# Kernel optimization log

Hardware: AMD Instinct MI355X
Metric: run time of the kernel (lower is better)

Reference implementation:

```python
import jax, jax.numpy as jnp
import numpy as np
from jax import lax

EPS = 1e-8

def squash(x, axis=-1):
    sq = jnp.sum(x * x, axis=axis, keepdims=True)
    return sq / (1.0 + sq) * x / (jnp.sqrt(sq) + EPS)

def setup_inputs() -> dict:
    key = jax.random.key(0)
    ks = jax.random.split(key, 12)
    B = 512
    x = jax.random.normal(ks[0], (B, 1, 28, 28), dtype=jnp.float32)
    conv1_w = 0.05 * jax.random.normal(ks[1], (256, 1, 9, 9), dtype=jnp.float32)
    conv1_b = jnp.zeros((256,), dtype=jnp.float32)
    prim_w = 0.01 * jax.random.normal(ks[2], (256, 256, 9, 9), dtype=jnp.float32)
    prim_b = jnp.zeros((256,), dtype=jnp.float32)
    # DigitCaps W: (out_caps=10, in_caps=1152, out_dim=16, in_dim=8)
    W_digit = 0.01 * jax.random.normal(ks[3], (10, 1152, 16, 8), dtype=jnp.float32)
    dec_w1 = 0.05 * jax.random.normal(ks[4], (512, 160), dtype=jnp.float32)
    dec_b1 = jnp.zeros((512,), dtype=jnp.float32)
    dec_w2 = 0.05 * jax.random.normal(ks[5], (1024, 512), dtype=jnp.float32)
    dec_b2 = jnp.zeros((1024,), dtype=jnp.float32)
    dec_w3 = 0.05 * jax.random.normal(ks[6], (784, 1024), dtype=jnp.float32)
    dec_b3 = jnp.zeros((784,), dtype=jnp.float32)
    return {"x": x, "conv1_w": conv1_w, "conv1_b": conv1_b,
            "prim_w": prim_w, "prim_b": prim_b, "W_digit": W_digit,
            "dec_w1": dec_w1, "dec_b1": dec_b1, "dec_w2": dec_w2,
            "dec_b2": dec_b2, "dec_w3": dec_w3, "dec_b3": dec_b3}

def reference(x, conv1_w, conv1_b, prim_w, prim_b, W_digit,
              dec_w1, dec_b1, dec_w2, dec_b2, dec_w3, dec_b3):
    NUM_ROUTING = 3
    # conv1 + relu: [B,1,28,28] -> [B,256,20,20]
    out = lax.conv(x, conv1_w, (1, 1), 'VALID') + conv1_b[None, :, None, None]
    out = jax.nn.relu(out)
    # primary caps conv: -> [B,256,6,6]
    out = lax.conv(out, prim_w, (2, 2), 'VALID') + prim_b[None, :, None, None]
    N, C, H, W = out.shape
    # [B,32,8,6,6] -> [B,32,6,6,8] -> [B,1152,8]
    out = out.reshape(N, 32, 8, H, W).transpose(0, 1, 3, 4, 2).reshape(N, -1, 8)
    u = squash(out)
    # u_hat: [B, out_caps=10, in_caps=1152, out_dim=16]
    u_hat = jnp.einsum('ocdi,bci->bocd', W_digit, u)
    tu = lax.stop_gradient(u_hat)
    b = jnp.zeros((N, 10, 1152, 1), dtype=u_hat.dtype)
    for _ in range(NUM_ROUTING - 1):
        c = jax.nn.softmax(b, axis=1)
        s = jnp.sum(c * tu, axis=2)            # [B,10,16]
        v = squash(s)
        b = b + jnp.einsum('bocd,bod->boc', tu, v)[..., None]
    c = jax.nn.softmax(b, axis=1)
    s = jnp.sum(c * u_hat, axis=2)
    v = squash(s)                               # [B,10,16]
    logits = jnp.linalg.norm(v, axis=-1)        # [B,10]
    pred = jax.nn.one_hot(jnp.argmax(logits, axis=1), 10, dtype=v.dtype)  # [B,10]
    masked = (v * pred[..., None]).reshape(N, -1)  # [B,160]
    h = jax.nn.relu(masked @ dec_w1.T + dec_b1)
    h = jax.nn.relu(h @ dec_w2.T + dec_b2)
    reconstruction = jax.nn.sigmoid(h @ dec_w3.T + dec_b3)  # [B,784]
    return (logits, reconstruction)
```

## Files before the change

### kernel.cpp

```cpp
#include <hip/hip_runtime.h>
#include <math.h>

typedef unsigned short u16;
typedef unsigned int u32;
typedef __attribute__((ext_vector_type(4))) float f32x4;
typedef __attribute__((ext_vector_type(4))) u32 u32x4;
typedef __attribute__((ext_vector_type(8))) short s16x8;
typedef __attribute__((ext_vector_type(8))) u16 u16x8;

__device__ __forceinline__ float bf2f(u16 h) { return __uint_as_float(((u32)h) << 16); }
__device__ __forceinline__ u16 f2bf(float f) {
    u32 u = __float_as_uint(f);
    return (u16)((u + 0x7FFFu + ((u >> 16) & 1u)) >> 16);
}
__device__ __forceinline__ void unpack8(u16x8 a, float* f) {
    const u32* p = (const u32*)&a;
#pragma unroll
    for (int k = 0; k < 4; ++k) {
        u32 w = p[k];
        f[2 * k] = __uint_as_float(w << 16);
        f[2 * k + 1] = __uint_as_float(w & 0xffff0000u);
    }
}

#define OFF_CONV1 0ull
#define OFF_CP    104857600ull
#define OFF_UHAT  0ull
#define OFF_U     188743680ull
#define OFF_WR    198180864ull
#define OFF_WB    208797696ull
#define OFF_W1T   211746816ull
#define OFF_MASK  211829760ull
#define OFF_H1    212157440ull
#define OFF_H2    213206016ull

#define GLDS16(SRC, DST) __builtin_amdgcn_global_load_lds( \
    (const __attribute__((address_space(1))) unsigned int*)(SRC), \
    (__attribute__((address_space(3))) unsigned int*)(DST), 16, 0, 0)

__global__ void k_w1t(const float* __restrict__ cw, float* __restrict__ w1t) {
    int k = blockIdx.x, t = threadIdx.x;
    w1t[k * 256 + t] = cw[t * 81 + k];
}

__global__ void k_wr(const float* __restrict__ pw, u16* __restrict__ wr) {
    int och = blockIdx.x, t = threadIdx.x;
    const float* src = pw + (och * 256 + t) * 81;
    u16* dst = wr + (size_t)och * 20736 + t;
    for (int kk = 0; kk < 81; ++kk) dst[kk * 256] = f2bf(src[kk]);
}

__global__ void k_wb(const float* __restrict__ w, u16* __restrict__ o) {
    int i = (blockIdx.x * 256 + threadIdx.x) * 8;
    u16x8 r;
#pragma unroll
    for (int j = 0; j < 8; ++j) r[j] = f2bf(w[i + j]);
    *(u16x8*)&o[i] = r;
}

__global__ __launch_bounds__(256) void k_conv1(const float* __restrict__ x,
                                               const float* __restrict__ w1t,
                                               const float* __restrict__ bias,
                                               u16* __restrict__ out) {
    int b = blockIdx.x / 20, y = blockIdx.x % 20, t = threadIdx.x;
    __shared__ float xs[252];
    if (t < 252) xs[t] = x[b * 784 + y * 28 + t];
    __syncthreads();
    float acc[20];
#pragma unroll
    for (int i = 0; i < 20; ++i) acc[i] = 0.f;
#pragma unroll
    for (int ky = 0; ky < 9; ++ky) {
        float xr[28];
#pragma unroll
        for (int i = 0; i < 28; ++i) xr[i] = xs[ky * 28 + i];
#pragma unroll
        for (int kx = 0; kx < 9; ++kx) {
            float wv = w1t[(ky * 9 + kx) * 256 + t];
#pragma unroll
            for (int ox = 0; ox < 20; ++ox) acc[ox] += wv * xr[ox + kx];
        }
    }
    float bv = bias[t];
    u16* op = out + ((size_t)(b * 20 + y) * 20) * 256 + t;
#pragma unroll
    for (int ox = 0; ox < 20; ++ox) {
        float f = fmaxf(acc[ox] + bv, 0.f);
        op[ox * 256] = f2bf(f);
    }
}

__global__ __launch_bounds__(256) void k_gemm(const u16* __restrict__ wr,
                                              const u16* __restrict__ cin,
                                              float* __restrict__ cp) {
    __shared__ __align__(16) u16 Al[128 * 64];
    __shared__ __align__(16) u16 Bl[128 * 64];
    int tid = threadIdx.x, lane = tid & 63, w = tid >> 6;
    int pix0 = blockIdx.x * 128, och0 = blockIdx.y * 128, q = blockIdx.z;
    int kbase = q * 5184;
    int slot = lane & 7;
    const char* ab[4];
    const char* bb[4];
#pragma unroll
    for (int j = 0; j < 4; ++j) {
        int r = w * 32 + j * 8 + (lane >> 3);
        int sl = slot ^ (r & 7);
        ab[j] = (const char*)wr + (size_t)(och0 + r) * 41472 + sl * 16;
        int p = pix0 + r, bi = p / 36, rr = p % 36, yy = rr / 6, xx = rr % 6;
        bb[j] = (const char*)cin + (size_t)((bi * 20 + 2 * yy) * 20 + 2 * xx) * 512 + sl * 16;
    }
    f32x4 acc[4][4];
#pragma unroll
    for (int i = 0; i < 4; ++i)
#pragma unroll
        for (int j = 0; j < 4; ++j) acc[i][j] = (f32x4){0.f, 0.f, 0.f, 0.f};
    int wm = (w & 1) * 64, wn = (w >> 1) * 64;

    for (int it = 0; it < 81; ++it) {
        int kk0 = kbase + it * 64;
        int kykx = kk0 >> 8, ic0 = kk0 & 255;
        int aoffu = kk0 * 2;
        int boffu = ((kykx / 9) * 20 + (kykx % 9)) * 512 + ic0 * 2;
#pragma unroll
        for (int j = 0; j < 4; ++j) {
            GLDS16(ab[j] + aoffu, &Al[(w * 32 + j * 8) * 64]);
            GLDS16(bb[j] + boffu, &Bl[(w * 32 + j * 8) * 64]);
        }
        __syncthreads();
#pragma unroll
        for (int s = 0; s < 2; ++s) {
            s16x8 af[4], bf[4];
#pragma unroll
            for (int f = 0; f < 4; ++f) {
                int m = wm + f * 16 + (lane & 15);
                int ch = ((s << 2) + (lane >> 4)) ^ (m & 7);
                af[f] = *(const s16x8*)&Al[m * 64 + ch * 8];
                int n = wn + f * 16 + (lane & 15);
                int ch2 = ((s << 2) + (lane >> 4)) ^ (n & 7);
                bf[f] = *(const s16x8*)&Bl[n * 64 + ch2 * 8];
            }
#pragma unroll
            for (int fm = 0; fm < 4; ++fm)
#pragma unroll
                for (int fn = 0; fn < 4; ++fn)
                    acc[fm][fn] = __builtin_amdgcn_mfma_f32_16x16x32_bf16(
                        af[fm], bf[fn], acc[fm][fn], 0, 0, 0);
        }
        __syncthreads();
    }
#pragma unroll
    for (int fm = 0; fm < 4; ++fm) {
        int och = och0 + wm + fm * 16 + (lane >> 4) * 4;
#pragma unroll
        for (int fn = 0; fn < 4; ++fn) {
            int pix = pix0 + wn + fn * 16 + (lane & 15);
            *(f32x4*)&cp[(((size_t)q * 18432 + pix) << 8) + och] = acc[fm][fn];
        }
    }
}

__global__ void k_squash(const float* __restrict__ cp, const float* __restrict__ pbias,
                         u16* __restrict__ u) {
    int idx = blockIdx.x * 256 + threadIdx.x;
    int pix = idx >> 5, g = idx & 31;
    size_t base = ((size_t)pix << 8) + g * 8;
    f32x4 s0 = {0.f, 0.f, 0.f, 0.f}, s1 = {0.f, 0.f, 0.f, 0.f};
#pragma unroll
    for (int q = 0; q < 4; ++q) {
        s0 += *(const f32x4*)&cp[q * 4718592ull + base];
        s1 += *(const f32x4*)&cp[q * 4718592ull + base + 4];
    }
    s0 += *(const f32x4*)&pbias[g * 8];
    s1 += *(const f32x4*)&pbias[g * 8 + 4];
    float sq = s0.x * s0.x + s0.y * s0.y + s0.z * s0.z + s0.w * s0.w +
               s1.x * s1.x + s1.y * s1.y + s1.z * s1.z + s1.w * s1.w;
    float scale = (sq / (1.f + sq)) / (sqrtf(sq) + 1e-8f);
    int b = pix / 36, cap = g * 36 + pix % 36;
    u16x8 r;
    r[0] = f2bf(s0.x * scale); r[1] = f2bf(s0.y * scale);
    r[2] = f2bf(s0.z * scale); r[3] = f2bf(s0.w * scale);
    r[4] = f2bf(s1.x * scale); r[5] = f2bf(s1.y * scale);
    r[6] = f2bf(s1.z * scale); r[7] = f2bf(s1.w * scale);
    *(u16x8*)&u[((size_t)b * 1152 + cap) * 8] = r;
}

__global__ __launch_bounds__(256) void k_uhat(const u16* __restrict__ u,
                                              const u16* __restrict__ wb,
                                              u32* __restrict__ uhp) {
    int o = blockIdx.x, cg = blockIdx.y, bq = blockIdx.z, t = threadIdx.x;
    __shared__ __align__(16) u16 wl[64 * 136];
    const u16* wsrc = wb + ((size_t)o * 1152 + cg * 64) * 128;
    for (int i = t; i < 1024; i += 256) {
        int row = i >> 4, j = i & 15;
        *(u16x8*)&wl[row * 136 + j * 8] = *(const u16x8*)&wsrc[i * 8];
    }
    __syncthreads();
    int bl = t >> 5, c2l = t & 31;
    const u16* w0p = &wl[(2 * c2l) * 136];
    const u16* w1p = &wl[(2 * c2l + 1) * 136];
    for (int bt = bq * 16; bt < bq * 16 + 16; ++bt) {
        int b = bt * 8 + bl;
        const u16x8* up = (const u16x8*)(u + ((size_t)b * 1152 + cg * 64 + 2 * c2l) * 8);
        float u0[8], u1[8];
        unpack8(up[0], u0);
        unpack8(up[1], u1);
        u32 outv[16];
#pragma unroll
        for (int d = 0; d < 16; ++d) {
            u16x8 wv0 = *(const u16x8*)&w0p[d * 8];
            u16x8 wv1 = *(const u16x8*)&w1p[d * 8];
            float w0f[8], w1f[8];
            unpack8(wv0, w0f);
            unpack8(wv1, w1f);
            float dA = 0.f, dB = 0.f;
#pragma unroll
            for (int i = 0; i < 8; ++i) {
                dA += w0f[i] * u0[i];
                dB += w1f[i] * u1[i];
            }
            outv[d] = (u32)f2bf(dA) | ((u32)f2bf(dB) << 16);
        }
        u32* dst = uhp + (size_t)b * 92160 + (cg * 32 + c2l) * 160 + o * 16;
#pragma unroll
        for (int k = 0; k < 4; ++k)
            *(u32x4*)&dst[k * 4] = *(u32x4*)&outv[k * 4];
    }
}

__global__ __launch_bounds__(256, 2) void k_routing(const u32* __restrict__ uhp,
                                                    float* __restrict__ logits,
                                                    float* __restrict__ masked) {
    int b = blockIdx.x, t = threadIdx.x;
    __shared__ float blog[10][1160];
    __shared__ __align__(16) u32 chunk[32 * 164];
    __shared__ float cwl[10][66];
    __shared__ float v[160];
    __shared__ float lg[10];
    __shared__ int am;
    for (int i = t; i < 11600; i += 256) ((float*)blog)[i] = 0.f;
    const u32* uh = uhp + (size_t)b * 92160;
    int o16 = t >> 4, d16 = t & 15;
    float s = 0.f;
    __syncthreads();

    if (t < 160) {
        const u32* p = uh + t;
#pragma unroll 8
        for (int c2 = 0; c2 < 576; ++c2) {
            u32 wv = p[c2 * 160];
            s += bf2f((u16)(wv & 0xffffu)) + bf2f((u16)(wv >> 16));
        }
        s *= 0.1f;
        float sq = s * s;
        sq += __shfl_xor(sq, 1, 16);
        sq += __shfl_xor(sq, 2, 16);
        sq += __shfl_xor(sq, 4, 16);
        sq += __shfl_xor(sq, 8, 16);
        float scale = (sq / (1.f + sq)) / (sqrtf(sq) + 1e-8f);
        v[t] = s * scale;
    }
    __syncthreads();

    for (int pass = 1; pass < 3; ++pass) {
        float snew = 0.f;
        for (int cg = 0; cg < 18; ++cg) {
            const u32x4* src4 = (const u32x4*)(uh + (size_t)cg * 5120);
#pragma unroll
            for (int k = 0; k < 5; ++k) {
                int idx4 = t + k * 256;
                int c2l = idx4 / 40, j4 = idx4 - c2l * 40;
                ((u32x4*)chunk)[c2l * 41 + j4] = src4[idx4];
            }
            __syncthreads();
#pragma unroll
            for (int jj = 0; jj < 2; ++jj) {
                int idx = t + jj * 256;
                if (idx < 320) {
                    int c2l = idx / 10, o = idx - c2l * 10;
                    const u32* row = &chunk[c2l * 164 + o * 16];
                    const float* vp = &v[o * 16];
                    float d0 = 0.f, d1 = 0.f;
#pragma unroll
                    for (int d = 0; d < 16; ++d) {
                        u32 wv = row[d];
                        float vv = vp[d];
                        d0 += __uint_as_float(wv << 16) * vv;
                        d1 += __uint_as_float(wv & 0xffff0000u) * vv;
                    }
                    int c2 = cg * 32 + c2l;
                    blog[o][2 * c2] += d0;
                    blog[o][2 * c2 + 1] += d1;
                }
            }
            __syncthreads();
            if (t < 64) {
                int c = cg * 64 + t;
                float bb[10], mx = -1e30f;
#pragma unroll
                for (int o = 0; o < 10; ++o) { bb[o] = blog[o][c]; mx = fmaxf(mx, bb[o]); }
                float sum = 0.f;
#pragma unroll
                for (int o = 0; o < 10; ++o) { bb[o] = __expf(bb[o] - mx); sum += bb[o]; }
                float rs = 1.f / sum;
#pragma unroll
                for (int o = 0; o < 10; ++o) cwl[o][t] = bb[o] * rs;
            }
            __syncthreads();
            if (t < 160) {
                const u32* col = &chunk[t];
                const float* cwp = &cwl[o16][0];
#pragma unroll 8
                for (int c2l = 0; c2l < 32; ++c2l) {
                    u32 wv = col[c2l * 164];
                    snew += __uint_as_float(wv << 16) * cwp[2 * c2l] +
                            __uint_as_float(wv & 0xffff0000u) * cwp[2 * c2l + 1];
                }
            }
            __syncthreads();
        }
        if (t < 160) {
            s = snew;
            float sq = s * s;
            sq += __shfl_xor(sq, 1, 16);
            sq += __shfl_xor(sq, 2, 16);
            sq += __shfl_xor(sq, 4, 16);
            sq += __shfl_xor(sq, 8, 16);
            float scale = (sq / (1.f + sq)) / (sqrtf(sq) + 1e-8f);
            v[t] = s * scale;
            if (d16 == 0 && pass == 2) {
                float sn = sqrtf(sq);
                float l = (sq / (1.f + sq)) * (sn / (sn + 1e-8f));
                lg[o16] = l;
                logits[b * 10 + o16] = l;
            }
        }
        __syncthreads();
    }
    if (t == 0) {
        float best = lg[0];
        int bi = 0;
#pragma unroll
        for (int o = 1; o < 10; ++o)
            if (lg[o] > best) { best = lg[o]; bi = o; }
        am = bi;
    }
    __syncthreads();
    if (t < 160) masked[b * 160 + t] = (o16 == am) ? v[t] : 0.f;
}

template <int K, int OUTDIM, int ACT>
__global__ __launch_bounds__(256) void k_dec(const float* __restrict__ in,
                                             const float* __restrict__ W,
                                             const float* __restrict__ bias,
                                             float* __restrict__ out) {
    int bt = blockIdx.y * 8;
    int o = blockIdx.x * 256 + threadIdx.x;
    __shared__ float ins[8 * K];
    for (int i = threadIdx.x; i < 8 * K; i += 256) ins[i] = in[(size_t)bt * K + i];
    __syncthreads();
    if (o < OUTDIM) {
        float acc[8];
#pragma unroll
        for (int bb = 0; bb < 8; ++bb) acc[bb] = 0.f;
        const float* wr = W + (size_t)o * K;
#pragma unroll 4
        for (int k = 0; k < K; ++k) {
            float wv = wr[k];
#pragma unroll
            for (int bb = 0; bb < 8; ++bb) acc[bb] += wv * ins[bb * K + k];
        }
        float bv = bias[o];
#pragma unroll
        for (int bb = 0; bb < 8; ++bb) {
            float z = acc[bb] + bv;
            float r = (ACT == 0) ? fmaxf(z, 0.f) : 1.f / (1.f + __expf(-z));
            out[(size_t)(bt + bb) * OUTDIM + o] = r;
        }
    }
}

extern "C" void kernel_launch(void* const* d_in, const int* in_sizes, int n_in,
                              void* d_out, int out_size, void* d_ws, size_t ws_size,
                              hipStream_t stream) {
    const float* x       = (const float*)d_in[0];
    const float* conv1_w = (const float*)d_in[1];
    const float* conv1_b = (const float*)d_in[2];
    const float* prim_w  = (const float*)d_in[3];
    const float* prim_b  = (const float*)d_in[4];
    const float* W_digit = (const float*)d_in[5];
    const float* dec_w1  = (const float*)d_in[6];
    const float* dec_b1  = (const float*)d_in[7];
    const float* dec_w2  = (const float*)d_in[8];
    const float* dec_b2  = (const float*)d_in[9];
    const float* dec_w3  = (const float*)d_in[10];
    const float* dec_b3  = (const float*)d_in[11];

    char* ws = (char*)d_ws;
    u16*   conv1o = (u16*)(ws + OFF_CONV1);
    float* cp     = (float*)(ws + OFF_CP);
    u32*   uhat   = (u32*)(ws + OFF_UHAT);
    u16*   u      = (u16*)(ws + OFF_U);
    u16*   wrq    = (u16*)(ws + OFF_WR);
    u16*   wb     = (u16*)(ws + OFF_WB);
    float* w1t    = (float*)(ws + OFF_W1T);
    float* maskd  = (float*)(ws + OFF_MASK);
    float* h1     = (float*)(ws + OFF_H1);
    float* h2     = (float*)(ws + OFF_H2);
    float* logits = (float*)d_out;
    float* recon  = (float*)d_out + 5120;

    k_w1t<<<dim3(81), dim3(256), 0, stream>>>(conv1_w, w1t);
    k_wr<<<dim3(256), dim3(256), 0, stream>>>(prim_w, wrq);
    k_wb<<<dim3(720), dim3(256), 0, stream>>>(W_digit, wb);
    k_conv1<<<dim3(10240), dim3(256), 0, stream>>>(x, w1t, conv1_b, conv1o);
    k_gemm<<<dim3(144, 2, 4), dim3(256), 0, stream>>>(wrq, conv1o, cp);
    k_squash<<<dim3(2304), dim3(256), 0, stream>>>(cp, prim_b, u);
    k_uhat<<<dim3(10, 18, 4), dim3(256), 0, stream>>>(u, wb, uhat);
    k_routing<<<dim3(512), dim3(256), 0, stream>>>(uhat, logits, maskd);
    k_dec<160, 512, 0><<<dim3(2, 64), dim3(256), 0, stream>>>(maskd, dec_w1, dec_b1, h1);
    k_dec<512, 1024, 0><<<dim3(4, 64), dim3(256), 0, stream>>>(h1, dec_w2, dec_b2, h2);
    k_dec<1024, 784, 1><<<dim3(4, 64), dim3(256), 0, stream>>>(h2, dec_w3, dec_b3, recon);
}
```

Baseline: 803.4 us.

## Double-buffer primary-caps GEMM LDS, halve split-K, and coalesce weight repack

The primary-caps GEMM now keeps two LDS buffers and issues the global-to-LDS loads for the next K-slice while MFMAs run on the current one, so load latency overlaps with compute. The split-K factor drops from 4 to 2: each block covers twice the K range, and squash reads and sums only two partial buffers, which cuts partial-sum write and read traffic. The weight repack kernel now stages through shared memory so both its global reads and writes are coalesced. The trade-offs are half as many GEMM blocks (576), which may leave CUs underused, and double the LDS per block (64KB), which limits occupancy.

```diff
diff --git a/kernel.cpp b/kernel.cpp
--- a/kernel.cpp
+++ b/kernel.cpp
@@ -43,11 +43,24 @@
     w1t[k * 256 + t] = cw[t * 81 + k];
 }
 
-__global__ void k_wr(const float* __restrict__ pw, u16* __restrict__ wr) {
+__global__ __launch_bounds__(256) void k_wr(const float* __restrict__ pw,
+                                            u16* __restrict__ wrq) {
     int och = blockIdx.x, t = threadIdx.x;
-    const float* src = pw + (och * 256 + t) * 81;
-    u16* dst = wr + (size_t)och * 20736 + t;
-    for (int kk = 0; kk < 81; ++kk) dst[kk * 256] = f2bf(src[kk]);
+    __shared__ u16 ld[128 * 82];
+    const float* src = pw + (size_t)och * 20736;
+    u16* dst = wrq + (size_t)och * 20736;
+    for (int half = 0; half < 2; ++half) {
+        const float* s2 = src + half * 128 * 81;
+        for (int i = t; i < 128 * 81; i += 256) {
+            int ic = i / 81, kk = i - ic * 81;
+            ld[ic * 82 + kk] = f2bf(s2[i]);
+        }
+        __syncthreads();
+        int col = t & 127, kh = t >> 7;
+        for (int kk = kh; kk < 81; kk += 2)
+            dst[kk * 256 + half * 128 + col] = ld[col * 82 + kk];
+        __syncthreads();
+    }
 }
 
 __global__ void k_wb(const float* __restrict__ w, u16* __restrict__ o) {
@@ -93,11 +106,11 @@
 __global__ __launch_bounds__(256) void k_gemm(const u16* __restrict__ wr,
                                               const u16* __restrict__ cin,
                                               float* __restrict__ cp) {
-    __shared__ __align__(16) u16 Al[128 * 64];
-    __shared__ __align__(16) u16 Bl[128 * 64];
+    __shared__ __align__(16) u16 Al[2][128 * 64];
+    __shared__ __align__(16) u16 Bl[2][128 * 64];
     int tid = threadIdx.x, lane = tid & 63, w = tid >> 6;
     int pix0 = blockIdx.x * 128, och0 = blockIdx.y * 128, q = blockIdx.z;
-    int kbase = q * 5184;
+    int kbase = q * 10368;
     int slot = lane & 7;
     const char* ab[4];
     const char* bb[4];
@@ -116,17 +129,23 @@
         for (int j = 0; j < 4; ++j) acc[i][j] = (f32x4){0.f, 0.f, 0.f, 0.f};
     int wm = (w & 1) * 64, wn = (w >> 1) * 64;
 
-    for (int it = 0; it < 81; ++it) {
+    auto stage = [&](int buf, int it) {
         int kk0 = kbase + it * 64;
         int kykx = kk0 >> 8, ic0 = kk0 & 255;
         int aoffu = kk0 * 2;
         int boffu = ((kykx / 9) * 20 + (kykx % 9)) * 512 + ic0 * 2;
 #pragma unroll
         for (int j = 0; j < 4; ++j) {
-            GLDS16(ab[j] + aoffu, &Al[(w * 32 + j * 8) * 64]);
-            GLDS16(bb[j] + boffu, &Bl[(w * 32 + j * 8) * 64]);
-        }
-        __syncthreads();
+            GLDS16(ab[j] + aoffu, &Al[buf][(w * 32 + j * 8) * 64]);
+            GLDS16(bb[j] + boffu, &Bl[buf][(w * 32 + j * 8) * 64]);
+        }
+    };
+
+    stage(0, 0);
+    __syncthreads();
+    int cur = 0;
+    for (int it = 0; it < 162; ++it) {
+        if (it + 1 < 162) stage(cur ^ 1, it + 1);
 #pragma unroll
         for (int s = 0; s < 2; ++s) {
             s16x8 af[4], bf[4];
@@ -134,10 +153,10 @@
             for (int f = 0; f < 4; ++f) {
                 int m = wm + f * 16 + (lane & 15);
                 int ch = ((s << 2) + (lane >> 4)) ^ (m & 7);
-                af[f] = *(const s16x8*)&Al[m * 64 + ch * 8];
+                af[f] = *(const s16x8*)&Al[cur][m * 64 + ch * 8];
                 int n = wn + f * 16 + (lane & 15);
                 int ch2 = ((s << 2) + (lane >> 4)) ^ (n & 7);
-                bf[f] = *(const s16x8*)&Bl[n * 64 + ch2 * 8];
+                bf[f] = *(const s16x8*)&Bl[cur][n * 64 + ch2 * 8];
             }
 #pragma unroll
             for (int fm = 0; fm < 4; ++fm)
@@ -147,6 +166,7 @@
                         af[fm], bf[fn], acc[fm][fn], 0, 0, 0);
         }
         __syncthreads();
+        cur ^= 1;
     }
 #pragma unroll
     for (int fm = 0; fm < 4; ++fm) {
@@ -166,7 +186,7 @@
     size_t base = ((size_t)pix << 8) + g * 8;
     f32x4 s0 = {0.f, 0.f, 0.f, 0.f}, s1 = {0.f, 0.f, 0.f, 0.f};
 #pragma unroll
-    for (int q = 0; q < 4; ++q) {
+    for (int q = 0; q < 2; ++q) {
         s0 += *(const f32x4*)&cp[q * 4718592ull + base];
         s1 += *(const f32x4*)&cp[q * 4718592ull + base + 4];
     }
@@ -413,7 +433,7 @@
     k_wr<<<dim3(256), dim3(256), 0, stream>>>(prim_w, wrq);
     k_wb<<<dim3(720), dim3(256), 0, stream>>>(W_digit, wb);
     k_conv1<<<dim3(10240), dim3(256), 0, stream>>>(x, w1t, conv1_b, conv1o);
-    k_gemm<<<dim3(144, 2, 4), dim3(256), 0, stream>>>(wrq, conv1o, cp);
+    k_gemm<<<dim3(144, 2, 2), dim3(256), 0, stream>>>(wrq, conv1o, cp);
     k_squash<<<dim3(2304), dim3(256), 0, stream>>>(cp, prim_b, u);
     k_uhat<<<dim3(10, 18, 4), dim3(256), 0, stream>>>(u, wb, uhat);
     k_routing<<<dim3(512), dim3(256), 0, stream>>>(uhat, logits, maskd);
```

Measured after the change: 869.9 us. 8.3% more time.
